# Optimization experiments

Measured on AMD Instinct MI355X. Metric: run time of the kernel, lower is better.

The kernel has to match this reference:

```python
import jax, jax.numpy as jnp
import numpy as np

S = 4  # MC samples


def _gat_layer(x, mask, w, a_src, a_dst, bias):
    # x: (b,n,fin)  w: (H,fin,fout)  mask: (b,n,n) bool
    h = jnp.einsum('bnf,hfo->bhno', x, w)                      # (b,H,n,fout)
    th = jnp.tanh(h)
    att_src = jnp.einsum('bhno,ho->bhn', th, a_src)
    att_dst = jnp.einsum('bhno,ho->bhn', th, a_dst)
    logits = jax.nn.leaky_relu(att_src[:, :, :, None] + att_dst[:, :, None, :], 0.2)
    logits = jnp.where(mask[:, None, :, :], logits, jnp.float32(-1e9))
    att = jax.nn.softmax(logits, axis=-1)                      # (b,H,n,n)
    out = jnp.einsum('bhij,bhjo->bhio', att, h) + bias         # (b,H,n,fout)
    return out, att


def setup_inputs() -> dict:
    key = jax.random.key(0)
    ks = jax.random.split(key, 11)
    b, n, f0, emb_d = 128, 128, 64, 64
    H1, f1, H2, f2 = 8, 16, 1, 2
    fin1 = f0 + emb_d            # 128 (n_units[0] += 64)
    fin2 = H1 * f1               # 128 (heads concatenated between layers)
    x = jax.random.normal(ks[0], (b, n, f0), jnp.float32)
    emb = jax.random.normal(ks[1], (b, n, emb_d), jnp.float32)
    adj = jax.random.randint(ks[2], (b, n, n), 0, 2).astype(jnp.int32)
    adj = jnp.maximum(adj, jnp.eye(n, dtype=jnp.int32)[None])  # self-loops keep softmax rows valid
    w1 = jax.random.normal(ks[3], (S, H1, fin1, f1), jnp.float32) * 0.1
    a_src1 = jax.random.normal(ks[4], (S, H1, f1), jnp.float32) * 0.1
    a_dst1 = jax.random.normal(ks[5], (S, H1, f1), jnp.float32) * 0.1
    b1 = jax.random.normal(ks[6], (f1,), jnp.float32) * 0.1
    w2 = jax.random.normal(ks[7], (S, H2, fin2, f2), jnp.float32) * 0.1
    a_src2 = jax.random.normal(ks[8], (S, H2, f2), jnp.float32) * 0.1
    a_dst2 = jax.random.normal(ks[9], (S, H2, f2), jnp.float32) * 0.1
    b2 = jax.random.normal(ks[10], (f2,), jnp.float32) * 0.1
    return dict(x=x, emb=emb, adj=adj, w1=w1, a_src1=a_src1, a_dst1=a_dst1, b1=b1,
                w2=w2, a_src2=a_src2, a_dst2=a_dst2, b2=b2)


def reference(x, emb, adj, w1, a_src1, a_dst1, b1, w2, a_src2, a_dst2, b2):
    mask = adj.astype(bool)
    x0 = jnp.concatenate([x, emb], axis=-1)                    # (b,n,128)
    b, n = x0.shape[0], x0.shape[1]
    xs = jnp.broadcast_to(x0, (S,) + x0.shape)                 # same input for each MC sample
    layer = jax.vmap(_gat_layer, in_axes=(0, None, 0, 0, 0, None))
    # layer 1 (per-sample variational weights), ELU activation
    h1, att1 = layer(xs, mask, w1, a_src1, a_dst1, b1)         # h1: (S,b,H1,n,f1)
    h1 = jax.nn.elu(h1)
    # concat heads: transpose(1,2).view(bs,n,-1)
    xs2 = jnp.transpose(h1, (0, 1, 3, 2, 4)).reshape(S, b, n, -1)
    # layer 2 (last layer): no activation, mean over heads
    h2, att2 = layer(xs2, mask, w2, a_src2, a_dst2, b2)        # (S,b,1,n,2)
    out = h2.mean(axis=2)                                      # (S,b,n,2)
    logp = jax.nn.log_softmax(out, axis=-1)[:, :, -1, :]       # (S,b,2) -> ego node
    result = jnp.mean(logp, axis=0)                            # var_mean -> mean (return_uncertainty=False)
    return result
```

## Files before the change

### kernel.cpp

```cpp
#include <hip/hip_runtime.h>
#include <stdint.h>
#include <math.h>

typedef __attribute__((ext_vector_type(8))) short short8;
typedef __attribute__((ext_vector_type(4))) float floatx4;

#define L_HF    0
#define L_SRC   16384
#define L_DST   18432
#define L_MASK  20480
#define L_H2P   22528
#define L_SIZE  26624

#define WS_H2_BYTES   (1024*256*4)

union F8 { short8 s8; uint32_t u[4]; };

#if __has_builtin(__builtin_amdgcn_exp2f)
#define EXP2F __builtin_amdgcn_exp2f
#else
#define EXP2F exp2f
#endif
#define LOG2E  1.4426950408889634f
#define LOG2E2 2.8853900817779268f

__device__ __forceinline__ uint32_t packbf(float a, float b){
  uint32_t ua = __float_as_uint(a), ub = __float_as_uint(b);
  uint32_t ra = (ua + 0x7fffu + ((ua>>16)&1u)) >> 16;
  uint32_t rb = (ub + 0x7fffu + ((ub>>16)&1u)) >> 16;
  return ra | (rb<<16);
}
__device__ __forceinline__ uint32_t packbf_t(float a, float b){
  return __builtin_amdgcn_perm(__float_as_uint(b), __float_as_uint(a), 0x07060302u);
}
__device__ __forceinline__ float fast_tanh(float x){
  float e = EXP2F(LOG2E2*x);
  return fmaf(-2.f, __builtin_amdgcn_rcpf(e + 1.f), 1.f);
}
__device__ __forceinline__ float mexp2(float l, uint32_t mb, int jj){
  float e = EXP2F(l);
  int sm = ((int)(mb << (31-jj))) >> 31;
  return __int_as_float(__float_as_int(e) & sm);
}
__device__ __forceinline__ float red16(float x){
  x += __int_as_float(__builtin_amdgcn_update_dpp(0, __float_as_int(x), 0x128, 0xf, 0xf, true));
  x += __int_as_float(__builtin_amdgcn_update_dpp(0, __float_as_int(x), 0x124, 0xf, 0xf, true));
  x += __int_as_float(__builtin_amdgcn_update_dpp(0, __float_as_int(x), 0x122, 0xf, 0xf, true));
  x += __int_as_float(__builtin_amdgcn_update_dpp(0, __float_as_int(x), 0x121, 0xf, 0xf, true));
  return x;
}

__global__ void mask_build(const int* __restrict__ adj, uint32_t* __restrict__ mask_ws) {
  const int t = threadIdx.x;
  const int row = blockIdx.x*4 + (t>>6);
  const int lane = t & 63;
  const int* ar = adj + (size_t)row*128;
  uint64_t m0 = __ballot(ar[lane] != 0);
  uint64_t m1 = __ballot(ar[64+lane] != 0);
  if (lane == 0) {
    ((uint4*)mask_ws)[row] = make_uint4((uint32_t)m0, (uint32_t)(m0>>32),
                                        (uint32_t)m1, (uint32_t)(m1>>32));
  }
}

__global__ __launch_bounds__(512,6) void gat_fused(
    const float* __restrict__ x,  const float* __restrict__ emb,
    const float* __restrict__ w1,
    const float* __restrict__ a_src1, const float* __restrict__ a_dst1,
    const float* __restrict__ b1, const float* __restrict__ w2,
    const uint32_t* __restrict__ mask_ws, float* __restrict__ ws_h2)
{
  __shared__ __align__(16) char smem[L_SIZE];
  char*     hf    = smem + L_HF;
  uint32_t* hf_u  = (uint32_t*)(smem + L_HF);
  float*    src_l = (float*)(smem + L_SRC);
  float*    dst_l = (float*)(smem + L_DST);
  uint32_t* mask_l= (uint32_t*)(smem + L_MASK);
  const uint4* mask4 = (const uint4*)(smem + L_MASK);
  float2*   h2p   = (float2*)(smem + L_H2P);

  const int t    = threadIdx.x;
  const int blk  = blockIdx.x;
  const int s    = blk >> 8;
  const int bb   = (blk & 255) >> 1;
  const int half = blk & 1;
  const int lane = t & 63, w = t >> 6;
  const int of = lane & 15, kg = lane >> 4;

  mask_l[t] = mask_ws[(size_t)bb*512 + t];

  const int arow = w*16 + of;
  const float* xrow = x   + ((size_t)bb*128 + arow)*64;
  const float* erow = emb + ((size_t)bb*128 + arow)*64;
  short8 af[4];
  #pragma unroll
  for (int ks=0; ks<4; ++ks){
    int k = ks*32 + kg*8;
    const float* p = (k<64) ? (xrow+k) : (erow + (k-64));
    float4 f0 = *(const float4*)p, f1 = *(const float4*)(p+4);
    F8 fr;
    fr.u[0]=packbf_t(f0.x,f0.y); fr.u[1]=packbf_t(f0.z,f0.w);
    fr.u[2]=packbf_t(f1.x,f1.y); fr.u[3]=packbf_t(f1.z,f1.w);
    af[ks]=fr.s8;
  }

  {
    const float* w1s = w1 + (size_t)s*16384 + half*8192;
    #pragma unroll
    for (int r=0; r<2; ++r){
      int q = t + r*512;
      int ql = q & 63, ks = (q>>6)&3, ct = q>>8;
      const float* wp = w1s + ct*2048 + (ks*32 + (ql>>4)*8)*16 + (ql&15);
      F8 fr;
      fr.u[0]=packbf_t(wp[0],  wp[16]);
      fr.u[1]=packbf_t(wp[32], wp[48]);
      fr.u[2]=packbf_t(wp[64], wp[80]);
      fr.u[3]=packbf_t(wp[96], wp[112]);
      *(short8*)(hf + ((ct*4+ks)*64 + ql)*16) = fr.s8;
    }
  }
  __syncthreads();

  floatx4 acc[4];
  #pragma unroll
  for (int ct=0; ct<4; ++ct) acc[ct]=(floatx4){0.f,0.f,0.f,0.f};
  #pragma unroll
  for (int ct=0; ct<4; ++ct)
    #pragma unroll
    for (int ks=0; ks<4; ++ks){
      short8 bfr = *(const short8*)(hf + ((ct*4+ks)*64 + lane)*16);
      acc[ct] = __builtin_amdgcn_mfma_f32_16x16x32_bf16(af[ks], bfr, acc[ct], 0,0,0);
    }
  __syncthreads();

  const int ks_h = w>>1, kgp = (w&1)*2 + (kg>>1), vv = (kg&1)*2;
  #pragma unroll
  for (int ct=0; ct<4; ++ct){
    const int ghd = half*4 + ct;
    float asv = a_src1[s*128 + ghd*16 + of] * LOG2E;
    float adv = a_dst1[s*128 + ghd*16 + of] * LOG2E;
    float ps[4], pd[4];
    #pragma unroll
    for (int r=0; r<4; ++r){
      float th = fast_tanh(acc[ct][r]);
      ps[r] = red16(th*asv); pd[r] = red16(th*adv);
    }
    if (of==0){
      #pragma unroll
      for (int r=0; r<4; ++r){
        int i = w*16 + kg*4 + r;
        src_l[ct*128+i]=ps[r]; dst_l[ct*128+i]=pd[r];
      }
    }
    uint32_t p0 = packbf(acc[ct][0], acc[ct][1]);
    uint32_t p1 = packbf(acc[ct][2], acc[ct][3]);
    uint32_t* dsth = hf_u + ((ct*4+ks_h)*64 + kgp*16 + of)*4 + vv;
    *(uint2*)dsth = make_uint2(p0, p1);
  }
  __syncthreads();

  const int lhd = w >> 1;
  const int ghd = half*4 + lhd;
  const int rtb = (w&1)*4;
  float b1v  = b1[of];
  float w2c0 = w2[s*256 + (ghd*16+of)*2 + 0];
  float w2c1 = w2[s*256 + (ghd*16+of)*2 + 1];
  F8 onesf;
  onesf.u[0]=0x3F803F80u; onesf.u[1]=0x3F803F80u;
  onesf.u[2]=0x3F803F80u; onesf.u[3]=0x3F803F80u;

  #pragma unroll
  for (int pp=0; pp<2; ++pp){
    const int rt0 = rtb + pp*2, rt1 = rt0 + 1;
    const int im0 = rt0*16 + of, im1 = rt1*16 + of;
    float srcv0 = src_l[lhd*128 + im0];
    float srcv1 = src_l[lhd*128 + im1];
    uint4 mrow0 = mask4[im0];
    uint4 mrow1 = mask4[im1];
    floatx4 acc20 = (floatx4){0.f,0.f,0.f,0.f};
    floatx4 acc21 = (floatx4){0.f,0.f,0.f,0.f};
    floatx4 accz0 = (floatx4){0.f,0.f,0.f,0.f};
    floatx4 accz1 = (floatx4){0.f,0.f,0.f,0.f};
    #pragma unroll
    for (int ks=0; ks<4; ++ks){
      const float* dp = dst_l + lhd*128 + ks*32 + kg*8;
      float4 d0 = *(const float4*)dp, d1 = *(const float4*)(dp+4);
      short8 hbk = *(const short8*)(hf + ((lhd*4+ks)*64 + lane)*16);
      uint32_t mw0 = (ks==0)?mrow0.x:(ks==1)?mrow0.y:(ks==2)?mrow0.z:mrow0.w;
      uint32_t mw1 = (ks==0)?mrow1.x:(ks==1)?mrow1.y:(ks==2)?mrow1.z:mrow1.w;
      uint32_t mb0 = mw0 >> (kg*8);
      uint32_t mb1 = mw1 >> (kg*8);
      float dj[8] = {d0.x,d0.y,d0.z,d0.w,d1.x,d1.y,d1.z,d1.w};
      F8 fr0, fr1;
      #pragma unroll
      for (int jp=0; jp<4; ++jp){
        const int j0 = 2*jp, j1 = 2*jp+1;
        float ta0 = srcv0 + dj[j0], ta1 = srcv0 + dj[j1];
        float tb0 = srcv1 + dj[j0], tb1 = srcv1 + dj[j1];
        float la0 = fmaxf(ta0, 0.2f*ta0), la1 = fmaxf(ta1, 0.2f*ta1);
        float lb0 = fmaxf(tb0, 0.2f*tb0), lb1 = fmaxf(tb1, 0.2f*tb1);
        float ea0 = mexp2(la0, mb0, j0), ea1 = mexp2(la1, mb0, j1);
        float eb0 = mexp2(lb0, mb1, j0), eb1 = mexp2(lb1, mb1, j1);
        fr0.u[jp] = packbf_t(ea0, ea1);
        fr1.u[jp] = packbf_t(eb0, eb1);
      }
      acc20 = __builtin_amdgcn_mfma_f32_16x16x32_bf16(fr0.s8, hbk,      acc20, 0,0,0);
      accz0 = __builtin_amdgcn_mfma_f32_16x16x32_bf16(fr0.s8, onesf.s8, accz0, 0,0,0);
      acc21 = __builtin_amdgcn_mfma_f32_16x16x32_bf16(fr1.s8, hbk,      acc21, 0,0,0);
      accz1 = __builtin_amdgcn_mfma_f32_16x16x32_bf16(fr1.s8, onesf.s8, accz1, 0,0,0);
    }
    #pragma unroll
    for (int pr=0; pr<2; ++pr){
      const int rt = pr ? rt1 : rt0;
      floatx4 a2 = pr ? acc21 : acc20;
      floatx4 az = pr ? accz1 : accz0;
      float pc0[4], pc1[4];
      #pragma unroll
      for (int r=0; r<4; ++r){
        float zi = __builtin_amdgcn_rcpf(az[r]);
        float o  = fmaf(a2[r], zi, b1v);
        float oe = (o>0.f) ? o : (__expf(o)-1.f);
        pc0[r] = red16(oe*w2c0);
        pc1[r] = red16(oe*w2c1);
      }
      if (of==0){
        #pragma unroll
        for (int r=0; r<4; ++r){
          int i = rt*16 + kg*4 + r;
          h2p[lhd*128 + i] = make_float2(pc0[r], pc1[r]);
        }
      }
    }
  }
  __syncthreads();

  if (t < 256){
    const int jn = t>>1, cc = t&1;
    float hv = 0.f;
    #pragma unroll
    for (int hd2=0; hd2<4; ++hd2){
      float2 p = h2p[hd2*128+jn];
      hv += cc ? p.y : p.x;
    }
    ws_h2[(size_t)blk*256 + t] = hv;
  }
}

__global__ __launch_bounds__(256) void gat_tail(
    const float* __restrict__ ws_h2, const int* __restrict__ adj,
    const float* __restrict__ a_src2, const float* __restrict__ a_dst2,
    const float* __restrict__ b2, float* __restrict__ out)
{
  __shared__ float d2_l[128];
  __shared__ float red[16];
  __shared__ float srcE;
  const int bb = blockIdx.x, t = threadIdx.x;
  const int jn = t>>1, cc = t&1, lane = t&63, w = t>>6;
  const uint32_t bit = (adj[((size_t)bb*128+127)*128 + jn] != 0) ? 1u : 0u;
  float acc0=0.f, acc1=0.f;
  for (int s=0; s<4; ++s){
    float hv = ws_h2[(size_t)(s*256 + bb*2 + 0)*256 + t]
             + ws_h2[(size_t)(s*256 + bb*2 + 1)*256 + t];
    float th2 = fast_tanh(hv);
    float ps2 = th2*a_src2[s*2+cc];
    float pd2 = th2*a_dst2[s*2+cc];
    ps2 += __shfl_xor(ps2,1);
    pd2 += __shfl_xor(pd2,1);
    if (s) __syncthreads();
    if (cc==0) d2_l[jn]=pd2;
    if (t==254) srcE=ps2;
    __syncthreads();
    float t0 = srcE + d2_l[jn];
    float lg = fmaxf(t0, 0.2f*t0);
    float v  = bit ? lg : -1e9f;
    float mloc = v;
    #pragma unroll
    for (int off=32; off>=1; off>>=1) mloc = fmaxf(mloc, __shfl_xor(mloc,off));
    if (lane==0) red[w]=mloc;
    __syncthreads();
    float M = fmaxf(fmaxf(red[0],red[1]), fmaxf(red[2],red[3]));
    float e2 = __expf(v-M);
    float vA = e2*hv;
    float vZ = (cc==0) ? e2 : 0.f;
    #pragma unroll
    for (int off=2; off<=32; off<<=1){ vA+=__shfl_xor(vA,off); vZ+=__shfl_xor(vZ,off); }
    if (lane==0){ red[4+w]=vA; red[12+w]=vZ; }
    if (lane==1){ red[8+w]=vA; }
    __syncthreads();
    if (t==0){
      float S0 = red[4]+red[5]+red[6]+red[7];
      float S1 = red[8]+red[9]+red[10]+red[11];
      float Z  = red[12]+red[13]+red[14]+red[15];
      float o0 = S0/Z + b2[0];
      float o1 = S1/Z + b2[1];
      float mm = fmaxf(o0,o1);
      float lse = mm + logf(__expf(o0-mm)+__expf(o1-mm));
      acc0 += 0.25f*(o0 - lse);
      acc1 += 0.25f*(o1 - lse);
    }
  }
  if (t==0){ out[bb*2+0]=acc0; out[bb*2+1]=acc1; }
}

extern "C" void kernel_launch(void* const* d_in, const int* in_sizes, int n_in,
                              void* d_out, int out_size, void* d_ws, size_t ws_size,
                              hipStream_t stream) {
  const float* x      = (const float*)d_in[0];
  const float* emb    = (const float*)d_in[1];
  const int*   adj    = (const int*)d_in[2];
  const float* w1     = (const float*)d_in[3];
  const float* a_src1 = (const float*)d_in[4];
  const float* a_dst1 = (const float*)d_in[5];
  const float* b1     = (const float*)d_in[6];
  const float* w2     = (const float*)d_in[7];
  const float* a_src2 = (const float*)d_in[8];
  const float* a_dst2 = (const float*)d_in[9];
  const float* b2     = (const float*)d_in[10];

  float*    ws_h2   = (float*)d_ws;
  uint32_t* mask_ws = (uint32_t*)((char*)d_ws + WS_H2_BYTES);

  mask_build<<<dim3(4096), dim3(256), 0, stream>>>(adj, mask_ws);
  gat_fused<<<dim3(1024), dim3(512), 0, stream>>>(x, emb, w1, a_src1, a_dst1,
                                                  b1, w2, mask_ws, ws_h2);
  gat_tail<<<dim3(128), dim3(256), 0, stream>>>(ws_h2, adj, a_src2, a_dst2, b2,
                                                (float*)d_out);
}
```

Baseline: 123.6 us.

## Fuse layer-2 tail into main kernel with one block per sample-graph

Each block now handles all 8 heads of one (sample, graph) pair instead of half of them. This doubles the shared memory and per-thread accumulators, and the launch-bounds occupancy hint drops from 6 to 4. The second-layer attention and log-softmax run inside the fused kernel on warp 0, with per-sample results combined through atomicAdd into an output zeroed by mask_build. This removes the third kernel launch and the workspace round-trip for h2. In exchange, grid parallelism halves, per-block work serializes over more row tiles, and occupancy may drop.

```diff
diff --git a/kernel.cpp b/kernel.cpp
--- a/kernel.cpp
+++ b/kernel.cpp
@@ -6,13 +6,11 @@
 typedef __attribute__((ext_vector_type(4))) float floatx4;
 
 #define L_HF    0
-#define L_SRC   16384
-#define L_DST   18432
-#define L_MASK  20480
-#define L_H2P   22528
-#define L_SIZE  26624
-
-#define WS_H2_BYTES   (1024*256*4)
+#define L_SRC   32768
+#define L_DST   36864
+#define L_MASK  40960
+#define L_H2P   43008
+#define L_SIZE  51200
 
 union F8 { short8 s8; uint32_t u[4]; };
 
@@ -50,8 +48,10 @@
   return x;
 }
 
-__global__ void mask_build(const int* __restrict__ adj, uint32_t* __restrict__ mask_ws) {
+__global__ void mask_build(const int* __restrict__ adj, uint32_t* __restrict__ mask_ws,
+                           float* __restrict__ out) {
   const int t = threadIdx.x;
+  if (blockIdx.x == 0 && t < 256) out[t] = 0.f;
   const int row = blockIdx.x*4 + (t>>6);
   const int lane = t & 63;
   const int* ar = adj + (size_t)row*128;
@@ -63,12 +63,14 @@
   }
 }
 
-__global__ __launch_bounds__(512,6) void gat_fused(
+__global__ __launch_bounds__(512,4) void gat_fused(
     const float* __restrict__ x,  const float* __restrict__ emb,
     const float* __restrict__ w1,
     const float* __restrict__ a_src1, const float* __restrict__ a_dst1,
     const float* __restrict__ b1, const float* __restrict__ w2,
-    const uint32_t* __restrict__ mask_ws, float* __restrict__ ws_h2)
+    const float* __restrict__ a_src2, const float* __restrict__ a_dst2,
+    const float* __restrict__ b2,
+    const uint32_t* __restrict__ mask_ws, float* __restrict__ out)
 {
   __shared__ __align__(16) char smem[L_SIZE];
   char*     hf    = smem + L_HF;
@@ -81,9 +83,8 @@
 
   const int t    = threadIdx.x;
   const int blk  = blockIdx.x;
-  const int s    = blk >> 8;
-  const int bb   = (blk & 255) >> 1;
-  const int half = blk & 1;
+  const int s    = blk >> 7;
+  const int bb   = blk & 127;
   const int lane = t & 63, w = t >> 6;
   const int of = lane & 15, kg = lane >> 4;
 
@@ -105,9 +106,9 @@
   }
 
   {
-    const float* w1s = w1 + (size_t)s*16384 + half*8192;
-    #pragma unroll
-    for (int r=0; r<2; ++r){
+    const float* w1s = w1 + (size_t)s*16384;
+    #pragma unroll
+    for (int r=0; r<4; ++r){
       int q = t + r*512;
       int ql = q & 63, ks = (q>>6)&3, ct = q>>8;
       const float* wp = w1s + ct*2048 + (ks*32 + (ql>>4)*8)*16 + (ql&15);
@@ -121,11 +122,11 @@
   }
   __syncthreads();
 
-  floatx4 acc[4];
+  floatx4 acc[8];
   #pragma unroll
-  for (int ct=0; ct<4; ++ct) acc[ct]=(floatx4){0.f,0.f,0.f,0.f};
+  for (int ct=0; ct<8; ++ct) acc[ct]=(floatx4){0.f,0.f,0.f,0.f};
   #pragma unroll
-  for (int ct=0; ct<4; ++ct)
+  for (int ct=0; ct<8; ++ct)
     #pragma unroll
     for (int ks=0; ks<4; ++ks){
       short8 bfr = *(const short8*)(hf + ((ct*4+ks)*64 + lane)*16);
@@ -135,10 +136,9 @@
 
   const int ks_h = w>>1, kgp = (w&1)*2 + (kg>>1), vv = (kg&1)*2;
   #pragma unroll
-  for (int ct=0; ct<4; ++ct){
-    const int ghd = half*4 + ct;
-    float asv = a_src1[s*128 + ghd*16 + of] * LOG2E;
-    float adv = a_dst1[s*128 + ghd*16 + of] * LOG2E;
+  for (int ct=0; ct<8; ++ct){
+    float asv = a_src1[s*128 + ct*16 + of] * LOG2E;
+    float adv = a_dst1[s*128 + ct*16 + of] * LOG2E;
     float ps[4], pd[4];
     #pragma unroll
     for (int r=0; r<4; ++r){
@@ -159,22 +159,20 @@
   }
   __syncthreads();
 
-  const int lhd = w >> 1;
-  const int ghd = half*4 + lhd;
-  const int rtb = (w&1)*4;
+  const int hd = w;
   float b1v  = b1[of];
-  float w2c0 = w2[s*256 + (ghd*16+of)*2 + 0];
-  float w2c1 = w2[s*256 + (ghd*16+of)*2 + 1];
+  float w2c0 = w2[s*256 + (hd*16+of)*2 + 0];
+  float w2c1 = w2[s*256 + (hd*16+of)*2 + 1];
   F8 onesf;
   onesf.u[0]=0x3F803F80u; onesf.u[1]=0x3F803F80u;
   onesf.u[2]=0x3F803F80u; onesf.u[3]=0x3F803F80u;
 
-  #pragma unroll
-  for (int pp=0; pp<2; ++pp){
-    const int rt0 = rtb + pp*2, rt1 = rt0 + 1;
+  #pragma unroll 2
+  for (int pp=0; pp<4; ++pp){
+    const int rt0 = pp*2, rt1 = rt0 + 1;
     const int im0 = rt0*16 + of, im1 = rt1*16 + of;
-    float srcv0 = src_l[lhd*128 + im0];
-    float srcv1 = src_l[lhd*128 + im1];
+    float srcv0 = src_l[hd*128 + im0];
+    float srcv1 = src_l[hd*128 + im1];
     uint4 mrow0 = mask4[im0];
     uint4 mrow1 = mask4[im1];
     floatx4 acc20 = (floatx4){0.f,0.f,0.f,0.f};
@@ -183,9 +181,9 @@
     floatx4 accz1 = (floatx4){0.f,0.f,0.f,0.f};
     #pragma unroll
     for (int ks=0; ks<4; ++ks){
-      const float* dp = dst_l + lhd*128 + ks*32 + kg*8;
+      const float* dp = dst_l + hd*128 + ks*32 + kg*8;
       float4 d0 = *(const float4*)dp, d1 = *(const float4*)(dp+4);
-      short8 hbk = *(const short8*)(hf + ((lhd*4+ks)*64 + lane)*16);
+      short8 hbk = *(const short8*)(hf + ((hd*4+ks)*64 + lane)*16);
       uint32_t mw0 = (ks==0)?mrow0.x:(ks==1)?mrow0.y:(ks==2)?mrow0.z:mrow0.w;
       uint32_t mw1 = (ks==0)?mrow1.x:(ks==1)?mrow1.y:(ks==2)?mrow1.z:mrow1.w;
       uint32_t mb0 = mw0 >> (kg*8);
@@ -227,79 +225,71 @@
         #pragma unroll
         for (int r=0; r<4; ++r){
           int i = rt*16 + kg*4 + r;
-          h2p[lhd*128 + i] = make_float2(pc0[r], pc1[r]);
+          h2p[hd*128 + i] = make_float2(pc0[r], pc1[r]);
         }
       }
     }
   }
   __syncthreads();
 
-  if (t < 256){
-    const int jn = t>>1, cc = t&1;
-    float hv = 0.f;
-    #pragma unroll
-    for (int hd2=0; hd2<4; ++hd2){
-      float2 p = h2p[hd2*128+jn];
-      hv += cc ? p.y : p.x;
-    }
-    ws_h2[(size_t)blk*256 + t] = hv;
-  }
-}
-
-__global__ __launch_bounds__(256) void gat_tail(
-    const float* __restrict__ ws_h2, const int* __restrict__ adj,
-    const float* __restrict__ a_src2, const float* __restrict__ a_dst2,
-    const float* __restrict__ b2, float* __restrict__ out)
-{
-  __shared__ float d2_l[128];
-  __shared__ float red[16];
-  __shared__ float srcE;
-  const int bb = blockIdx.x, t = threadIdx.x;
-  const int jn = t>>1, cc = t&1, lane = t&63, w = t>>6;
-  const uint32_t bit = (adj[((size_t)bb*128+127)*128 + jn] != 0) ? 1u : 0u;
-  float acc0=0.f, acc1=0.f;
-  for (int s=0; s<4; ++s){
-    float hv = ws_h2[(size_t)(s*256 + bb*2 + 0)*256 + t]
-             + ws_h2[(size_t)(s*256 + bb*2 + 1)*256 + t];
-    float th2 = fast_tanh(hv);
-    float ps2 = th2*a_src2[s*2+cc];
-    float pd2 = th2*a_dst2[s*2+cc];
-    ps2 += __shfl_xor(ps2,1);
-    pd2 += __shfl_xor(pd2,1);
-    if (s) __syncthreads();
-    if (cc==0) d2_l[jn]=pd2;
-    if (t==254) srcE=ps2;
-    __syncthreads();
-    float t0 = srcE + d2_l[jn];
-    float lg = fmaxf(t0, 0.2f*t0);
-    float v  = bit ? lg : -1e9f;
-    float mloc = v;
-    #pragma unroll
-    for (int off=32; off>=1; off>>=1) mloc = fmaxf(mloc, __shfl_xor(mloc,off));
-    if (lane==0) red[w]=mloc;
-    __syncthreads();
-    float M = fmaxf(fmaxf(red[0],red[1]), fmaxf(red[2],red[3]));
-    float e2 = __expf(v-M);
-    float vA = e2*hv;
-    float vZ = (cc==0) ? e2 : 0.f;
-    #pragma unroll
-    for (int off=2; off<=32; off<<=1){ vA+=__shfl_xor(vA,off); vZ+=__shfl_xor(vZ,off); }
-    if (lane==0){ red[4+w]=vA; red[12+w]=vZ; }
-    if (lane==1){ red[8+w]=vA; }
-    __syncthreads();
-    if (t==0){
-      float S0 = red[4]+red[5]+red[6]+red[7];
-      float S1 = red[8]+red[9]+red[10]+red[11];
-      float Z  = red[12]+red[13]+red[14]+red[15];
+  if (w == 0){
+    float hv[2][2];
+    #pragma unroll
+    for (int jj=0; jj<2; ++jj){
+      const int j = lane + jj*64;
+      float s0 = 0.f, s1 = 0.f;
+      #pragma unroll
+      for (int h2i=0; h2i<8; ++h2i){
+        float2 p = h2p[h2i*128 + j];
+        s0 += p.x; s1 += p.y;
+      }
+      hv[jj][0] = s0; hv[jj][1] = s1;
+    }
+    const float as0 = a_src2[s*2+0], as1 = a_src2[s*2+1];
+    const float ad0 = a_dst2[s*2+0], ad1 = a_dst2[s*2+1];
+    float ps1v = 0.f, pd[2];
+    #pragma unroll
+    for (int jj=0; jj<2; ++jj){
+      float th0 = fast_tanh(hv[jj][0]);
+      float th1 = fast_tanh(hv[jj][1]);
+      float psj = th0*as0 + th1*as1;
+      pd[jj]    = th0*ad0 + th1*ad1;
+      if (jj==1) ps1v = psj;
+    }
+    const float srcE = __shfl(ps1v, 63);
+    const uint32_t mwA = mask_l[127*4 + (lane>>5)];
+    const uint32_t mwB = mask_l[127*4 + 2 + (lane>>5)];
+    const int bitpos = lane & 31;
+    float v[2];
+    #pragma unroll
+    for (int jj=0; jj<2; ++jj){
+      float t0 = srcE + pd[jj];
+      float lg = fmaxf(t0, 0.2f*t0);
+      uint32_t mb = jj ? mwB : mwA;
+      v[jj] = ((mb >> bitpos) & 1u) ? lg : -1e9f;
+    }
+    float M = fmaxf(v[0], v[1]);
+    #pragma unroll
+    for (int off=32; off>=1; off>>=1) M = fmaxf(M, __shfl_xor(M, off));
+    float e0 = __expf(v[0]-M), e1 = __expf(v[1]-M);
+    float Z  = e0 + e1;
+    float S0 = e0*hv[0][0] + e1*hv[1][0];
+    float S1 = e0*hv[0][1] + e1*hv[1][1];
+    #pragma unroll
+    for (int off=32; off>=1; off>>=1){
+      Z  += __shfl_xor(Z,  off);
+      S0 += __shfl_xor(S0, off);
+      S1 += __shfl_xor(S1, off);
+    }
+    if (lane == 0){
       float o0 = S0/Z + b2[0];
       float o1 = S1/Z + b2[1];
       float mm = fmaxf(o0,o1);
       float lse = mm + logf(__expf(o0-mm)+__expf(o1-mm));
-      acc0 += 0.25f*(o0 - lse);
-      acc1 += 0.25f*(o1 - lse);
-    }
-  }
-  if (t==0){ out[bb*2+0]=acc0; out[bb*2+1]=acc1; }
+      atomicAdd(out + bb*2 + 0, 0.25f*(o0 - lse));
+      atomicAdd(out + bb*2 + 1, 0.25f*(o1 - lse));
+    }
+  }
 }
 
 extern "C" void kernel_launch(void* const* d_in, const int* in_sizes, int n_in,
@@ -317,12 +307,10 @@
   const float* a_dst2 = (const float*)d_in[9];
   const float* b2     = (const float*)d_in[10];
 
-  float*    ws_h2   = (float*)d_ws;
-  uint32_t* mask_ws = (uint32_t*)((char*)d_ws + WS_H2_BYTES);
-
-  mask_build<<<dim3(4096), dim3(256), 0, stream>>>(adj, mask_ws);
-  gat_fused<<<dim3(1024), dim3(512), 0, stream>>>(x, emb, w1, a_src1, a_dst1,
-                                                  b1, w2, mask_ws, ws_h2);
-  gat_tail<<<dim3(128), dim3(256), 0, stream>>>(ws_h2, adj, a_src2, a_dst2, b2,
-                                                (float*)d_out);
-}
+  uint32_t* mask_ws = (uint32_t*)d_ws;
+
+  mask_build<<<dim3(4096), dim3(256), 0, stream>>>(adj, mask_ws, (float*)d_out);
+  gat_fused<<<dim3(512), dim3(512), 0, stream>>>(x, emb, w1, a_src1, a_dst1, b1,
+                                                 w2, a_src2, a_dst2, b2,
+                                                 mask_ws, (float*)d_out);
+}
```

After: 118.1 us. 1.05x faster.
